# Optimization experiments

Measured on AMD Instinct MI355X. Metric: run time of the kernel, lower is better.

The kernel has to match this reference:

```python
import math
import jax, jax.numpy as jnp
import numpy as np

B, S, H, NH, BS, R = 2, 4096, 1024, 16, 64, 3
HD = H // NH          # 64 head dim
L = S // BS           # 64 blocks
PEN = -10000.0


def _make_rand_attn():
    # data-independent random block plan (like HF bigbird, seeded numpy),
    # per head, per middle query block: R random key blocks excluding
    # global blocks (0, L-1) and the sliding window (i-1, i, i+1)
    rng = np.random.RandomState(42)
    ra = np.zeros((NH, L - 2, R), dtype=np.int64)
    for h in range(NH):
        for i in range(1, L - 1):
            choices = np.array([j for j in range(L) if j not in (0, i - 1, i, i + 1, L - 1)])
            ra[h, i - 1] = rng.choice(choices, R, replace=False)
    return ra


def setup_inputs():
    key = jax.random.key(0)
    ks = jax.random.split(key, 8)
    sc = 1.0 / math.sqrt(H)
    return {
        "Q": jax.random.normal(ks[0], (B, S, H), jnp.float32),
        "K": jax.random.normal(ks[1], (B, S, H), jnp.float32),
        "V": jax.random.normal(ks[2], (B, S, H), jnp.float32),
        "mask": jnp.ones((B, S), jnp.float32),
        "Wq": jax.random.normal(ks[3], (H, H), jnp.float32) * sc,
        "bq": jnp.zeros((H,), jnp.float32),
        "Wk": jax.random.normal(ks[4], (H, H), jnp.float32) * sc,
        "bk": jnp.zeros((H,), jnp.float32),
        "Wv": jax.random.normal(ks[5], (H, H), jnp.float32) * sc,
        "bv": jnp.zeros((H,), jnp.float32),
        "rand_attn": jnp.asarray(_make_rand_attn()),
    }


def _forward(Q, K, V, mask, Wq, bq, Wk, bk, Wv, bv, rand_attn):
    rsd = 1.0 / math.sqrt(HD)
    sm = lambda x: jax.nn.softmax(x, axis=-1)

    def proj(x, W, b):  # torch Linear: x @ W^T + b, then split heads
        return (x @ W.T + b).reshape(B, S, NH, HD).transpose(0, 2, 1, 3)

    q = proj(Q, Wq, bq)  # [B,NH,S,HD]
    k = proj(K, Wk, bk)
    v = proj(V, Wv, bv)
    qb = q.reshape(B, NH, L, BS, HD)
    kb = k.reshape(B, NH, L, BS, HD)
    vb = v.reshape(B, NH, L, BS, HD)

    # ---- masks (derived from padding mask, as in HF create_masks_...) ----
    blocked = mask.reshape(B, L, BS)
    from_mask = mask[:, None, :, None]   # [B,1,S,1]
    to_mask = mask[:, None, None, :]     # [B,1,1,S]
    exp_to = jnp.concatenate([blocked[:, 1:-3], blocked[:, 2:-2], blocked[:, 3:-1]], axis=2)  # [B,L-4,3BS]
    band_mask = jnp.einsum('blq,blk->blqk', blocked[:, 2:-2], exp_to)[:, None]  # [B,1,L-4,BS,3BS]

    ra = jnp.broadcast_to(rand_attn[None], (B, NH, L - 2, R))
    bidx = jnp.arange(B)[:, None, None, None]
    hidx = jnp.arange(NH)[None, :, None, None]
    gk = kb[bidx, hidx, ra].reshape(B, NH, L - 2, R * BS, HD)  # gathered random key blocks
    gv = vb[bidx, hidx, ra].reshape(B, NH, L - 2, R * BS, HD)
    rm = blocked[bidx, ra].reshape(B, NH, L - 2, R * BS)
    rand_mask = jnp.einsum('blq,bhlk->bhlqk', blocked[:, 1:-1], rm)  # [B,NH,L-2,BS,R*BS]

    # ---- first block: dense attention over all keys ----
    p1 = jnp.einsum('bhqd,bhkd->bhqk', qb[:, :, 0], k) * rsd + (1.0 - to_mask) * PEN
    ctx_first = jnp.einsum('bhqk,bhkd->bhqd', sm(p1), v)

    # ---- second block: global(0) + window(1,2) + last + random ----
    k2 = jnp.concatenate([kb[:, :, 0], kb[:, :, 1], kb[:, :, 2], kb[:, :, -1], gk[:, :, 0]], axis=2)
    v2 = jnp.concatenate([vb[:, :, 0], vb[:, :, 1], vb[:, :, 2], vb[:, :, -1], gv[:, :, 0]], axis=2)
    p2 = jnp.einsum('bhqd,bhkd->bhqk', qb[:, :, 1], k2) * rsd
    seq_pad2 = jnp.concatenate([to_mask[..., :3 * BS], to_mask[..., -BS:],
                                jnp.ones((B, 1, 1, R * BS), mask.dtype)], axis=3)
    rand_pad2 = jnp.concatenate([jnp.ones((B, NH, BS, 4 * BS), mask.dtype), rand_mask[:, :, 0]], axis=3)
    p2 = p2 + (1.0 - jnp.minimum(seq_pad2, rand_pad2)) * PEN
    ctx_second = jnp.einsum('bhqk,bhkd->bhqd', sm(p2), v2)

    # ---- middle blocks: band (3 sliding) + random + 2 global ----
    exp_k = jnp.concatenate([kb[:, :, 1:-3], kb[:, :, 2:-2], kb[:, :, 3:-1]], axis=3)  # [B,NH,L-4,3BS,HD]
    exp_v = jnp.concatenate([vb[:, :, 1:-3], vb[:, :, 2:-2], vb[:, :, 3:-1]], axis=3)
    mq = qb[:, :, 2:-2]
    inner = jnp.einsum('bhlqd,bhlkd->bhlqk', mq, exp_k) * rsd + (1.0 - band_mask) * PEN
    randp = jnp.einsum('bhlqd,bhlkd->bhlqk', mq, gk[:, :, 1:-1]) * rsd + (1.0 - rand_mask[:, :, 1:-1]) * PEN
    firstp = jnp.einsum('bhlqd,bhkd->bhlqk', mq, kb[:, :, 0]) * rsd + (1.0 - to_mask[:, :, :, None, :BS]) * PEN
    lastp = jnp.einsum('bhlqd,bhkd->bhlqk', mq, kb[:, :, -1]) * rsd + (1.0 - to_mask[:, :, :, None, -BS:]) * PEN
    w = sm(jnp.concatenate([firstp, inner, randp, lastp], axis=-1))  # [B,NH,L-4,BS,(5+R)*BS]
    ctx_mid = jnp.einsum('bhlqk,bhlkd->bhlqd', w[..., BS:4 * BS], exp_v)
    ctx_mid += jnp.einsum('bhlqk,bhlkd->bhlqd', w[..., 4 * BS:(4 + R) * BS], gv[:, :, 1:-1])
    ctx_mid += jnp.einsum('bhlqk,bhkd->bhlqd', w[..., :BS], vb[:, :, 0])
    ctx_mid += jnp.einsum('bhlqk,bhkd->bhlqd', w[..., -BS:], vb[:, :, -1])

    # ---- second-to-last block ----
    k3 = jnp.concatenate([kb[:, :, 0], kb[:, :, -3], kb[:, :, -2], kb[:, :, -1], gk[:, :, -1]], axis=2)
    v3 = jnp.concatenate([vb[:, :, 0], vb[:, :, -3], vb[:, :, -2], vb[:, :, -1], gv[:, :, -1]], axis=2)
    p3 = jnp.einsum('bhqd,bhkd->bhqk', qb[:, :, -2], k3) * rsd
    seq_pad3 = jnp.concatenate([to_mask[..., :BS], to_mask[..., -3 * BS:],
                                jnp.ones((B, 1, 1, R * BS), mask.dtype)], axis=3)
    rand_pad3 = jnp.concatenate([jnp.ones((B, NH, BS, 4 * BS), mask.dtype), rand_mask[:, :, -1]], axis=3)
    p3 = p3 + (1.0 - jnp.minimum(seq_pad3, rand_pad3)) * PEN
    ctx_seclast = jnp.einsum('bhqk,bhkd->bhqd', sm(p3), v3)

    # ---- last block: dense attention over all keys ----
    p4 = jnp.einsum('bhqd,bhkd->bhqk', qb[:, :, -1], k) * rsd + (1.0 - to_mask) * PEN
    ctx_last = jnp.einsum('bhqk,bhkd->bhqd', sm(p4), v)

    ctx = jnp.concatenate([ctx_first[:, :, None], ctx_second[:, :, None], ctx_mid,
                           ctx_seclast[:, :, None], ctx_last[:, :, None]], axis=2)
    ctx = ctx.reshape(B, NH, S, HD) * from_mask
    return ctx.transpose(0, 2, 1, 3).reshape(B, S, NH * HD)


def reference(Q, K, V, mask, Wq, bq, Wk, bk, Wv, bv, rand_attn):
    return _forward(Q, K, V, mask, Wq, bq, Wk, bk, Wv, bv, rand_attn)
```

## Files before the change

kernel.cpp:

```cpp
#include <hip/hip_runtime.h>
#include <hip/hip_bf16.h>
#include <stdint.h>

#define BB 2
#define SS 4096
#define HH 1024
#define NHh 16
#define HD 64
#define LL 64
#define BS 64
#define RR 3
#define PENf (-10000.0f)

typedef unsigned int uint;
typedef __attribute__((ext_vector_type(8))) short bf16x8;
typedef __attribute__((ext_vector_type(4))) float f32x4;

__device__ __forceinline__ ushort f2bf(float f) {
    union { float f; uint u; } v; v.f = f;
    uint u = v.u;
    return (ushort)((u + 0x7fffu + ((u >> 16) & 1u)) >> 16);
}
__device__ __forceinline__ uint pack_bf(float a, float b) {
    return (uint)f2bf(a) | (((uint)f2bf(b)) << 16);
}
__device__ __forceinline__ uint scale_pair(uint w) {
    float lo = __uint_as_float(w << 16) * 0.125f;
    float hi = __uint_as_float(w & 0xffff0000u) * 0.125f;
    return (uint)f2bf(lo) | (((uint)f2bf(hi)) << 16);
}
__device__ __forceinline__ uint4 scale4(uint4 w) {
    uint4 o;
    o.x = scale_pair(w.x); o.y = scale_pair(w.y);
    o.z = scale_pair(w.z); o.w = scale_pair(w.w);
    return o;
}
__device__ __forceinline__ void async16(const ushort* g, ushort* l) {
    __builtin_amdgcn_global_load_lds((const __attribute__((address_space(1))) uint*)g,
                                     (__attribute__((address_space(3))) uint*)l,
                                     16, 0, 0);
}

__global__ __launch_bounds__(256)
void cvt_kernel(const float* __restrict__ Xq, const float* __restrict__ Xk,
                const float* __restrict__ Xv, const float* __restrict__ Wq,
                const float* __restrict__ Wk, const float* __restrict__ Wv,
                ushort* __restrict__ Xbf, ushort* __restrict__ Wbf)
{
    const size_t XTOT = (size_t)3 * BB * SS * HH;
    const uint u = blockIdx.x * 256 + threadIdx.x;
    const size_t e = (size_t)u * 8;
    const float* src; ushort* dst;
    if (e < XTOT) {
        const int zz = (int)(e >> 23);
        src = (zz == 0 ? Xq : zz == 1 ? Xk : Xv) + (e & ((1u << 23) - 1));
        dst = Xbf + e;
    } else {
        const size_t e2 = e - XTOT;
        const int zz = (int)(e2 >> 20);
        src = (zz == 0 ? Wq : zz == 1 ? Wk : Wv) + (e2 & ((1u << 20) - 1));
        dst = Wbf + e2;
    }
    float4 a = ((const float4*)src)[0];
    float4 c = ((const float4*)src)[1];
    uint4 o;
    o.x = pack_bf(a.x, a.y); o.y = pack_bf(a.z, a.w);
    o.z = pack_bf(c.x, c.y); o.w = pack_bf(c.z, c.w);
    *(uint4*)dst = o;
}

__global__ __launch_bounds__(256)
void gemm3_kernel(const ushort* __restrict__ Xbf, const ushort* __restrict__ Wbf,
                  const float* __restrict__ bq, const float* __restrict__ bk,
                  const float* __restrict__ bv,
                  ushort* __restrict__ qb, ushort* __restrict__ kb,
                  ushort* __restrict__ vbT)
{
    __shared__ __align__(16) ushort smem[128 * 136];
    ushort* As = smem;
    ushort* Bs = smem + 8192;

    const int z = blockIdx.z;
    const ushort* A  = Xbf + (size_t)z * ((size_t)BB * SS * HH);
    const ushort* Bt = Wbf + (size_t)z * (HH * HH);
    const float* bias = (z == 0) ? bq : (z == 1) ? bk : bv;

    const int tid = threadIdx.x;
    const int m0 = blockIdx.x * 128;
    const int n0 = blockIdx.y * 128;
    const int wave = tid >> 6;
    const int lane = tid & 63;
    const int l15 = lane & 15;
    const int quad = lane >> 4;
    const int wr = wave >> 1, wc = wave & 1;

    f32x4 acc[4][4];
#pragma unroll
    for (int i = 0; i < 4; ++i)
#pragma unroll
        for (int j = 0; j < 4; ++j) acc[i][j] = (f32x4){0.f, 0.f, 0.f, 0.f};

    const int p8 = (lane & 3) * 8;
    const ushort* Abase = A + (size_t)(m0 + wave * 32 + (lane >> 2)) * HH + p8;
    const ushort* Bbase = Bt + (size_t)(n0 + wave * 32 + (lane >> 2)) * HH + p8;

#define STAGE_G(k0, bp)                                        \
    do {                                                       \
        ushort* A0 = As + (bp) * 4096 + wave * 1024;           \
        ushort* B0 = Bs + (bp) * 4096 + wave * 1024;           \
        async16(Abase + (k0), A0);                             \
        async16(Abase + 16 * HH + (k0), A0 + 512);             \
        async16(Bbase + (k0), B0);                             \
        async16(Bbase + 16 * HH + (k0), B0 + 512);             \
    } while (0)

    STAGE_G(0, 0);
    for (int k0 = 0, bp = 0; k0 < HH; k0 += 32, bp ^= 1) {
        __syncthreads();
        if (k0 + 32 < HH) STAGE_G(k0 + 32, bp ^ 1);
        bf16x8 af[4], bfr[4];
#pragma unroll
        for (int mt = 0; mt < 4; ++mt)
            af[mt] = *(const bf16x8*)(As + bp * 4096 + (wr * 64 + mt * 16 + l15) * 32 + quad * 8);
#pragma unroll
        for (int nt = 0; nt < 4; ++nt)
            bfr[nt] = *(const bf16x8*)(Bs + bp * 4096 + (wc * 64 + nt * 16 + l15) * 32 + quad * 8);
        if (z < 2) {
#pragma unroll
            for (int i = 0; i < 4; ++i)
#pragma unroll
                for (int j = 0; j < 4; ++j)
                    acc[i][j] = __builtin_amdgcn_mfma_f32_16x16x32_bf16(bfr[i], af[j], acc[i][j], 0, 0, 0);
        } else {
#pragma unroll
            for (int i = 0; i < 4; ++i)
#pragma unroll
                for (int j = 0; j < 4; ++j)
                    acc[i][j] = __builtin_amdgcn_mfma_f32_16x16x32_bf16(af[i], bfr[j], acc[i][j], 0, 0, 0);
        }
    }
#undef STAGE_G

    if (z < 2) {
        ushort* outp = (z == 0) ? qb : kb;
#pragma unroll
        for (int wt = 0; wt < 4; ++wt) {
            const int n_base = n0 + wc * 64 + wt * 16 + quad * 4;
            const float4 b4 = *(const float4*)&bias[n_base];
            const int nh = n_base >> 6;
            const int hd = n_base & 63;
#pragma unroll
            for (int xt = 0; xt < 4; ++xt) {
                const int m = m0 + wr * 64 + xt * 16 + l15;
                const int bgl = m >> 12, s = m & 4095;
                uint2 pk;
                pk.x = pack_bf(acc[wt][xt][0] + b4.x, acc[wt][xt][1] + b4.y);
                pk.y = pack_bf(acc[wt][xt][2] + b4.z, acc[wt][xt][3] + b4.w);
                *(uint2*)&outp[((size_t)((bgl << 4) | nh) * SS + s) * HD + hd] = pk;
            }
        }
    } else {
        __syncthreads();
        ushort* stg = smem;
#pragma unroll
        for (int nt = 0; nt < 4; ++nt) {
            const int n_local = wc * 64 + nt * 16 + l15;
            const float bn = bias[n0 + n_local];
#pragma unroll
            for (int mt = 0; mt < 4; ++mt) {
                const int m_base = wr * 64 + mt * 16 + quad * 4;
                uint2 pk;
                pk.x = pack_bf(acc[mt][nt][0] + bn, acc[mt][nt][1] + bn);
                pk.y = pack_bf(acc[mt][nt][2] + bn, acc[mt][nt][3] + bn);
                *(uint2*)(stg + n_local * 136 + m_base) = pk;
            }
        }
        __syncthreads();
        const int n_row = tid >> 1;
        const int half = tid & 1;
        const int n = n0 + n_row;
        const int nh = n >> 6, hd = n & 63;
        const int bgl = m0 >> 12;
        const int sbase = (m0 & 4095) + half * 64;
        const uint4* src = (const uint4*)(stg + n_row * 136 + half * 64);
        uint4* dst = (uint4*)(vbT + ((size_t)((bgl << 4) | nh) * HD + hd) * SS + sbase);
#pragma unroll
        for (int j = 0; j < 8; ++j) dst[j] = src[j];
    }
}

__global__ __launch_bounds__(256)
void proj3_kernel(const float* __restrict__ Xq, const float* __restrict__ Xk,
                  const float* __restrict__ Xv,
                  const float* __restrict__ Wq, const float* __restrict__ Wk,
                  const float* __restrict__ Wv,
                  const float* __restrict__ bq, const float* __restrict__ bk,
                  const float* __restrict__ bv,
                  ushort* __restrict__ qb, ushort* __restrict__ kb,
                  ushort* __restrict__ vbT)
{
    __shared__ __align__(16) ushort smem[128 * 136];
    ushort* As = smem;
    ushort* Bs = smem + 128 * 40;

    const int z = blockIdx.z;
    const float* X    = (z == 0) ? Xq : (z == 1) ? Xk : Xv;
    const float* W    = (z == 0) ? Wq : (z == 1) ? Wk : Wv;
    const float* bias = (z == 0) ? bq : (z == 1) ? bk : bv;

    const int tid = threadIdx.x;
    const int m0 = blockIdx.x * 128;
    const int n0 = blockIdx.y * 128;
    const int wave = tid >> 6;
    const int lane = tid & 63;
    const int l15 = lane & 15;
    const int quad = lane >> 4;
    const int wr = wave >> 1, wc = wave & 1;

    f32x4 acc[4][4];
#pragma unroll
    for (int mt = 0; mt < 4; ++mt)
#pragma unroll
        for (int nt = 0; nt < 4; ++nt) acc[mt][nt] = (f32x4){0.f, 0.f, 0.f, 0.f};

    const int srow = tid >> 1;
    const int shalf = tid & 1;
    const float* xp = X + (size_t)(m0 + srow) * HH + shalf * 16;
    const float* wp = W + (size_t)(n0 + srow) * HH + shalf * 16;
    ushort* asw = As + srow * 40 + shalf * 16;
    ushort* bsw = Bs + srow * 40 + shalf * 16;

    for (int k0 = 0; k0 < HH; k0 += 32) {
        float4 a0 = *(const float4*)(xp + k0);
        float4 a1 = *(const float4*)(xp + k0 + 4);
        float4 a2 = *(const float4*)(xp + k0 + 8);
        float4 a3 = *(const float4*)(xp + k0 + 12);
        float4 b0 = *(const float4*)(wp + k0);
        float4 b1 = *(const float4*)(wp + k0 + 4);
        float4 b2 = *(const float4*)(wp + k0 + 8);
        float4 b3 = *(const float4*)(wp + k0 + 12);
        __syncthreads();
        uint4 pa, pb;
        pa.x = pack_bf(a0.x, a0.y); pa.y = pack_bf(a0.z, a0.w);
        pa.z = pack_bf(a1.x, a1.y); pa.w = pack_bf(a1.z, a1.w);
        *(uint4*)asw = pa;
        pa.x = pack_bf(a2.x, a2.y); pa.y = pack_bf(a2.z, a2.w);
        pa.z = pack_bf(a3.x, a3.y); pa.w = pack_bf(a3.z, a3.w);
        *(uint4*)(asw + 8) = pa;
        pb.x = pack_bf(b0.x, b0.y); pb.y = pack_bf(b0.z, b0.w);
        pb.z = pack_bf(b1.x, b1.y); pb.w = pack_bf(b1.z, b1.w);
        *(uint4*)bsw = pb;
        pb.x = pack_bf(b2.x, b2.y); pb.y = pack_bf(b2.z, b2.w);
        pb.z = pack_bf(b3.x, b3.y); pb.w = pack_bf(b3.z, b3.w);
        *(uint4*)(bsw + 8) = pb;
        __syncthreads();

        bf16x8 af[4], bfr[4];
#pragma unroll
        for (int mt = 0; mt < 4; ++mt)
            af[mt] = *(const bf16x8*)(As + (wr * 64 + mt * 16 + l15) * 40 + quad * 8);
#pragma unroll
        for (int nt = 0; nt < 4; ++nt)
            bfr[nt] = *(const bf16x8*)(Bs + (wc * 64 + nt * 16 + l15) * 40 + quad * 8);
#pragma unroll
        for (int mt = 0; mt < 4; ++mt)
#pragma unroll
            for (int nt = 0; nt < 4; ++nt)
                acc[mt][nt] = __builtin_amdgcn_mfma_f32_16x16x32_bf16(af[mt], bfr[nt], acc[mt][nt], 0, 0, 0);
    }

    if (z < 2) {
        ushort* outp = (z == 0) ? qb : kb;
#pragma unroll
        for (int nt = 0; nt < 4; ++nt) {
            const int n = n0 + wc * 64 + nt * 16 + l15;
            const float bn = bias[n];
            const int nh = n >> 6, hd = n & 63;
#pragma unroll
            for (int mt = 0; mt < 4; ++mt) {
#pragma unroll
                for (int rr = 0; rr < 4; ++rr) {
                    const int m = m0 + wr * 64 + mt * 16 + quad * 4 + rr;
                    const int bgl = m >> 12, s = m & 4095;
                    outp[((size_t)((bgl << 4) | nh) * SS + s) * HD + hd] = f2bf(acc[mt][nt][rr] + bn);
                }
            }
        }
    } else {
        __syncthreads();
        ushort* stg = smem;
#pragma unroll
        for (int nt = 0; nt < 4; ++nt) {
            const int n_local = wc * 64 + nt * 16 + l15;
            const float bn = bias[n0 + n_local];
#pragma unroll
            for (int mt = 0; mt < 4; ++mt) {
                const int m_base = wr * 64 + mt * 16 + quad * 4;
                uint2 pk;
                pk.x = pack_bf(acc[mt][nt][0] + bn, acc[mt][nt][1] + bn);
                pk.y = pack_bf(acc[mt][nt][2] + bn, acc[mt][nt][3] + bn);
                *(uint2*)(stg + n_local * 136 + m_base) = pk;
            }
        }
        __syncthreads();
        const int n_row = tid >> 1;
        const int half = tid & 1;
        const int n = n0 + n_row;
        const int nh = n >> 6, hd = n & 63;
        const int bgl = m0 >> 12;
        const int sbase = (m0 & 4095) + half * 64;
        const uint4* src = (const uint4*)(stg + n_row * 136 + half * 64);
        uint4* dst = (uint4*)(vbT + ((size_t)((bgl << 4) | nh) * HD + hd) * SS + sbase);
#pragma unroll
        for (int j = 0; j < 8; ++j) dst[j] = src[j];
    }
}

__global__ __launch_bounds__(256)
void attn_kernel(const ushort* __restrict__ qg, const ushort* __restrict__ kg,
                 const ushort* __restrict__ vTg,
                 const float* __restrict__ mask, const int* __restrict__ rand_attn,
                 float* __restrict__ out, float* __restrict__ partO,
                 float* __restrict__ partML)
{
    __shared__ __align__(16) ushort qs_ps[64][72];
    __shared__ __align__(16) ushort ks2[2][2][64][32];
    __shared__ __align__(16) ushort vs2[2][2][64][32];
    __shared__ __align__(16) float qm_s[64];
    __shared__ __align__(16) float km_s[2][64];

    const int tid = threadIdx.x;
    const int wid = blockIdx.x;
    const int bh = wid / 78;
    const int r = wid - bh * 78;
    const int b = bh >> 4, h = bh & 15;

    int i, nkb;
    int kbl[8], pfl[8];
    bool dense;
    int part = 0, which = 0;
    if (r < 62) {
        dense = false;
        i = r + 1;
        const int* ra = rand_attn + ((size_t)h * (LL - 2) + (i - 1)) * RR;
        if (i == 1) {
            kbl[0] = 0; kbl[1] = 1; kbl[2] = 2; kbl[3] = LL - 1;
            kbl[4] = ra[0]; kbl[5] = ra[1]; kbl[6] = ra[2]; kbl[7] = 0;
            pfl[0] = pfl[1] = pfl[2] = pfl[3] = 0;
            pfl[4] = pfl[5] = pfl[6] = 1; pfl[7] = 0;
            nkb = 7;
        } else if (i == LL - 2) {
            kbl[0] = 0; kbl[1] = LL - 3; kbl[2] = LL - 2; kbl[3] = LL - 1;
            kbl[4] = ra[0]; kbl[5] = ra[1]; kbl[6] = ra[2]; kbl[7] = 0;
            pfl[0] = pfl[1] = pfl[2] = pfl[3] = 0;
            pfl[4] = pfl[5] = pfl[6] = 1; pfl[7] = 0;
            nkb = 7;
        } else {
            kbl[0] = 0;      pfl[0] = 0;
            kbl[1] = i - 1;  pfl[1] = 1;
            kbl[2] = i;      pfl[2] = 1;
            kbl[3] = i + 1;  pfl[3] = 1;
            kbl[4] = LL - 1; pfl[4] = 0;
            kbl[5] = ra[0]; kbl[6] = ra[1]; kbl[7] = ra[2];
            pfl[5] = pfl[6] = pfl[7] = 1;
            nkb = 8;
        }
    } else {
        dense = true;
        const int r2 = r - 62;
        which = r2 >> 3;
        part = r2 & 7;
        i = which ? (LL - 1) : 0;
        nkb = 8;
#pragma unroll
        for (int j = 0; j < 8; ++j) { kbl[j] = part * 8 + j; pfl[j] = 0; }
    }

    const int lane = tid & 63;
    const int wave = tid >> 6;
    const int l15 = lane & 15;
    const int quad = lane >> 4;
    const int srow = lane >> 2;
    const int p8 = (lane & 3) * 8;
    const ushort* kgb = kg + (size_t)bh * SS * HD;
    const ushort* vgb = vTg + (size_t)bh * HD * SS;

#define STAGE_KV(kb_, bp)                                                        \
    do {                                                                         \
        const size_t krow = (size_t)((kb_) * BS + wave * 16 + srow) * HD;        \
        async16(kgb + krow + p8,      &ks2[bp][0][wave * 16][0]);                \
        async16(kgb + krow + 32 + p8, &ks2[bp][1][wave * 16][0]);                \
        const size_t vrow = (size_t)(wave * 16 + srow) * SS + (kb_) * BS;        \
        async16(vgb + vrow + p8,      &vs2[bp][0][wave * 16][0]);                \
        async16(vgb + vrow + 32 + p8, &vs2[bp][1][wave * 16][0]);                \
    } while (0)

    {
        const int row = tid >> 2;
        const int c0 = (tid & 3) * 16;
        const ushort* src = qg + ((size_t)bh * SS + i * BS + row) * HD + c0;
        uint4 w0 = *(const uint4*)src;
        uint4 w1 = *(const uint4*)(src + 8);
        *(uint4*)&qs_ps[row][c0] = scale4(w0);
        *(uint4*)&qs_ps[row][c0 + 8] = scale4(w1);
        if (tid < 64) qm_s[tid] = mask[(size_t)b * SS + i * BS + tid];
    }
    STAGE_KV(kbl[0], 0);
    if (tid < 64) km_s[0][tid] = mask[(size_t)b * SS + kbl[0] * BS + tid];
    __syncthreads();

    bf16x8 aq[2];
    aq[0] = *(const bf16x8*)&qs_ps[wave * 16 + l15][quad * 8];
    aq[1] = *(const bf16x8*)&qs_ps[wave * 16 + l15][32 + quad * 8];
    const float qm = qm_s[wave * 16 + l15];

    float mrow = -1e30f, lrow = 0.0f;
    f32x4 accO[4];
#pragma unroll
    for (int dt = 0; dt < 4; ++dt) accO[dt] = (f32x4){0.f, 0.f, 0.f, 0.f};

    for (int it = 0; it < nkb; ++it) {
        const int cur = it & 1;
        if (it + 1 < nkb) {
            STAGE_KV(kbl[it + 1], cur ^ 1);
            if (tid < 64) km_s[cur ^ 1][tid] = mask[(size_t)b * SS + kbl[it + 1] * BS + tid];
        }
        const int pf = pfl[it];

        f32x4 sc[4];
#pragma unroll
        for (int nt = 0; nt < 4; ++nt) sc[nt] = (f32x4){0.f, 0.f, 0.f, 0.f};
#pragma unroll
        for (int c = 0; c < 2; ++c) {
#pragma unroll
            for (int nt = 0; nt < 4; ++nt) {
                bf16x8 af = *(const bf16x8*)&ks2[cur][c][nt * 16 + l15][quad * 8];
                sc[nt] = __builtin_amdgcn_mfma_f32_16x16x32_bf16(af, aq[c], sc[nt], 0, 0, 0);
            }
        }

        float p[4][4];
        float bm = -1e30f;
#pragma unroll
        for (int nt = 0; nt < 4; ++nt) {
            const float4 km4 = *(const float4*)&km_s[cur][nt * 16 + quad * 4];
            const float kmv[4] = {km4.x, km4.y, km4.z, km4.w};
#pragma unroll
            for (int rr = 0; rr < 4; ++rr) {
                const float pm = pf ? (qm * kmv[rr]) : kmv[rr];
                const float sv = sc[nt][rr] + (1.0f - pm) * PENf;
                p[nt][rr] = sv;
                bm = fmaxf(bm, sv);
            }
        }
        bm = fmaxf(bm, __shfl_xor(bm, 16));
        bm = fmaxf(bm, __shfl_xor(bm, 32));
        const float mn = fmaxf(mrow, bm);
        const float alpha = __expf(mrow - mn);
        mrow = mn;
        float ls = 0.0f;
#pragma unroll
        for (int nt = 0; nt < 4; ++nt)
#pragma unroll
            for (int rr = 0; rr < 4; ++rr) {
                p[nt][rr] = __expf(p[nt][rr] - mn);
                ls += p[nt][rr];
            }
        ls += __shfl_xor(ls, 16);
        ls += __shfl_xor(ls, 32);
        lrow = lrow * alpha + ls;

#pragma unroll
        for (int nt = 0; nt < 4; ++nt) {
            uint2 pk;
            pk.x = pack_bf(p[nt][0], p[nt][1]);
            pk.y = pack_bf(p[nt][2], p[nt][3]);
            *(uint2*)&qs_ps[wave * 16 + l15][nt * 16 + quad * 4] = pk;
        }
        float a4[4];
#pragma unroll
        for (int rr = 0; rr < 4; ++rr) a4[rr] = __shfl(alpha, quad * 4 + rr, 64);
#pragma unroll
        for (int dt = 0; dt < 4; ++dt) {
#pragma unroll
            for (int rr = 0; rr < 4; ++rr) accO[dt][rr] *= a4[rr];
        }

#pragma unroll
        for (int c = 0; c < 2; ++c) {
            bf16x8 ap = *(const bf16x8*)&qs_ps[wave * 16 + l15][c * 32 + quad * 8];
#pragma unroll
            for (int dt = 0; dt < 4; ++dt) {
                bf16x8 bvf = *(const bf16x8*)&vs2[cur][c][dt * 16 + l15][quad * 8];
                accO[dt] = __builtin_amdgcn_mfma_f32_16x16x32_bf16(ap, bvf, accO[dt], 0, 0, 0);
            }
        }

        if (it + 1 < nkb) __syncthreads();
    }
#undef STAGE_KV

    if (!dense) {
#pragma unroll
        for (int rr = 0; rr < 4; ++rr) {
            const int qloc = quad * 4 + rr;
            const float lq = __shfl(lrow, qloc, 64);
            const float inv = qm_s[wave * 16 + qloc] / lq;
#pragma unroll
            for (int dt = 0; dt < 4; ++dt) {
                const int d = dt * 16 + l15;
                out[((size_t)b * SS + i * BS + wave * 16 + qloc) * HH + h * HD + d] = accO[dt][rr] * inv;
            }
        }
    } else {
        const int slot = (bh * 2 + which) * 8 + part;
        float* po = partO + (size_t)slot * 4096;
#pragma unroll
        for (int rr = 0; rr < 4; ++rr) {
            const int qrow = wave * 16 + quad * 4 + rr;
#pragma unroll
            for (int dt = 0; dt < 4; ++dt) {
                const int d = dt * 16 + l15;
                po[qrow * 64 + d] = accO[dt][rr];
            }
        }
        if (lane < 16) {
            partML[slot * 128 + wave * 16 + lane] = mrow;
            partML[slot * 128 + 64 + wave * 16 + lane] = lrow;
        }
    }
}

__global__ __launch_bounds__(256)
void combine_kernel(const float* __restrict__ partO, const float* __restrict__ partML,
                    const float* __restrict__ mask, float* __restrict__ out)
{
    const int g = blockIdx.x;
    const int bh = g >> 1, which = g & 1;
    const int b = bh >> 4, h = bh & 15;
    const int i = which ? (LL - 1) : 0;
    const int t = threadIdx.x;
    const int row = t >> 2;
    const int d0 = (t & 3) * 16;
    const int base = g * 8;

    float mp[8], lp[8];
    float M = -1e30f;
#pragma unroll
    for (int p = 0; p < 8; ++p) {
        mp[p] = partML[(base + p) * 128 + row];
        lp[p] = partML[(base + p) * 128 + 64 + row];
        M = fmaxf(M, mp[p]);
    }
    float L = 0.0f, w[8];
#pragma unroll
    for (int p = 0; p < 8; ++p) { w[p] = __expf(mp[p] - M); L += lp[p] * w[p]; }

    float4 o[4];
#pragma unroll
    for (int j = 0; j < 4; ++j) o[j] = make_float4(0.f, 0.f, 0.f, 0.f);
#pragma unroll
    for (int p = 0; p < 8; ++p) {
        const float* po = partO + (size_t)(base + p) * 4096 + row * 64 + d0;
#pragma unroll
        for (int j = 0; j < 4; ++j) {
            float4 v = *(const float4*)(po + j * 4);
            o[j].x = fmaf(w[p], v.x, o[j].x);
            o[j].y = fmaf(w[p], v.y, o[j].y);
            o[j].z = fmaf(w[p], v.z, o[j].z);
            o[j].w = fmaf(w[p], v.w, o[j].w);
        }
    }
    const float fm = mask[(size_t)b * SS + i * BS + row];
    const float inv = fm / L;
    float* dst = out + ((size_t)b * SS + i * BS + row) * HH + h * HD + d0;
#pragma unroll
    for (int j = 0; j < 4; ++j) {
        float4 v;
        v.x = o[j].x * inv; v.y = o[j].y * inv;
        v.z = o[j].z * inv; v.w = o[j].w * inv;
        *(float4*)(dst + j * 4) = v;
    }
}

extern "C" void kernel_launch(void* const* d_in, const int* in_sizes, int n_in,
                              void* d_out, int out_size, void* d_ws, size_t ws_size,
                              hipStream_t stream) {
    (void)in_sizes; (void)n_in; (void)out_size;
    const float* Q    = (const float*)d_in[0];
    const float* K    = (const float*)d_in[1];
    const float* V    = (const float*)d_in[2];
    const float* mask = (const float*)d_in[3];
    const float* Wq   = (const float*)d_in[4];
    const float* bq   = (const float*)d_in[5];
    const float* Wk   = (const float*)d_in[6];
    const float* bk   = (const float*)d_in[7];
    const float* Wv   = (const float*)d_in[8];
    const float* bv   = (const float*)d_in[9];
    const int*   ra   = (const int*)d_in[10];
    float* out = (float*)d_out;

    const size_t qkv = (size_t)BB * NHh * SS * HD;
    ushort* qb  = (ushort*)d_ws;
    ushort* kb  = qb + qkv;
    ushort* vbT = kb + qkv;
    float* partO  = (float*)(vbT + qkv);
    float* partML = partO + (size_t)512 * 4096;
    ushort* Xbf = (ushort*)(partML + (size_t)512 * 128);
    ushort* Wbf = Xbf + 3 * qkv;
    const size_t need = (size_t)((char*)(Wbf + (size_t)3 * HH * HH) - (char*)d_ws);

    if (ws_size >= need) {
        cvt_kernel<<<13824, 256, 0, stream>>>(Q, K, V, Wq, Wk, Wv, Xbf, Wbf);
        gemm3_kernel<<<dim3(64, 8, 3), 256, 0, stream>>>(Xbf, Wbf, bq, bk, bv, qb, kb, vbT);
    } else {
        proj3_kernel<<<dim3(64, 8, 3), 256, 0, stream>>>(Q, K, V, Wq, Wk, Wv, bq, bk, bv,
                                                         qb, kb, vbT);
    }
    attn_kernel<<<dim3(BB * NHh * 78), 256, 0, stream>>>(qb, kb, vbT, mask, ra,
                                                         out, partO, partML);
    combine_kernel<<<dim3(BB * NHh * 2), 256, 0, stream>>>(partO, partML, mask, out);
}
```

Measured before the change: 303.5 us.

## Fuse split-K combine into attention via atomic counter; use exp2 and MFMA row-sums

Folds log2(e) into the Q scale and the mask penalty so the softmax can use exp2f, and turns the mask add into a single fma seeded into the MFMA accumulator. Row sums come from an extra MFMA against a ones vector instead of shuffle reductions. The separate combine kernel is removed on the main path: the last partial block of each dense row group, detected with an atomic counter reset in cvt_kernel, does the merge itself. This saves one launch and some VALU work, at the cost of a threadfence, an atomic, and a serialized tail combine inside the attention kernel.

```diff
diff --git a/kernel.cpp b/kernel.cpp
--- a/kernel.cpp
+++ b/kernel.cpp
@@ -11,6 +11,8 @@
 #define BS 64
 #define RR 3
 #define PENf (-10000.0f)
+#define PEN2f (-14426.950408889634f)
+#define QSCALE (0.125f * 1.44269504088896f)
 
 typedef unsigned int uint;
 typedef __attribute__((ext_vector_type(8))) short bf16x8;
@@ -25,8 +27,8 @@
     return (uint)f2bf(a) | (((uint)f2bf(b)) << 16);
 }
 __device__ __forceinline__ uint scale_pair(uint w) {
-    float lo = __uint_as_float(w << 16) * 0.125f;
-    float hi = __uint_as_float(w & 0xffff0000u) * 0.125f;
+    float lo = __uint_as_float(w << 16) * QSCALE;
+    float hi = __uint_as_float(w & 0xffff0000u) * QSCALE;
     return (uint)f2bf(lo) | (((uint)f2bf(hi)) << 16);
 }
 __device__ __forceinline__ uint4 scale4(uint4 w) {
@@ -45,8 +47,10 @@
 void cvt_kernel(const float* __restrict__ Xq, const float* __restrict__ Xk,
                 const float* __restrict__ Xv, const float* __restrict__ Wq,
                 const float* __restrict__ Wk, const float* __restrict__ Wv,
-                ushort* __restrict__ Xbf, ushort* __restrict__ Wbf)
+                ushort* __restrict__ Xbf, ushort* __restrict__ Wbf,
+                int* __restrict__ ctr)
 {
+    if (blockIdx.x == 0 && threadIdx.x < 64) ctr[threadIdx.x] = 0;
     const size_t XTOT = (size_t)3 * BB * SS * HH;
     const uint u = blockIdx.x * 256 + threadIdx.x;
     const size_t e = (size_t)u * 8;
@@ -321,7 +325,7 @@
                  const ushort* __restrict__ vTg,
                  const float* __restrict__ mask, const int* __restrict__ rand_attn,
                  float* __restrict__ out, float* __restrict__ partO,
-                 float* __restrict__ partML)
+                 float* __restrict__ partML, int* __restrict__ ctr, int fused)
 {
     __shared__ __align__(16) ushort qs_ps[64][72];
     __shared__ __align__(16) ushort ks2[2][2][64][32];
@@ -413,9 +417,19 @@
     aq[0] = *(const bf16x8*)&qs_ps[wave * 16 + l15][quad * 8];
     aq[1] = *(const bf16x8*)&qs_ps[wave * 16 + l15][32 + quad * 8];
     const float qm = qm_s[wave * 16 + l15];
-
-    float mrow = -1e30f, lrow = 0.0f;
+    const float a_pf = qm * (-PEN2f);
+    const float a_nf = -PEN2f;
+
+    bf16x8 ones;
+    {
+        const short ob = (l15 == 0) ? (short)0x3F80 : (short)0;
+#pragma unroll
+        for (int j = 0; j < 8; ++j) ones[j] = ob;
+    }
+
+    float mrow = -1e30f;
     f32x4 accO[4];
+    f32x4 accL = (f32x4){0.f, 0.f, 0.f, 0.f};
 #pragma unroll
     for (int dt = 0; dt < 4; ++dt) accO[dt] = (f32x4){0.f, 0.f, 0.f, 0.f};
 
@@ -429,7 +443,7 @@
 
         f32x4 sc[4];
 #pragma unroll
-        for (int nt = 0; nt < 4; ++nt) sc[nt] = (f32x4){0.f, 0.f, 0.f, 0.f};
+        for (int nt = 0; nt < 4; ++nt) sc[nt] = (f32x4){PEN2f, PEN2f, PEN2f, PEN2f};
 #pragma unroll
         for (int c = 0; c < 2; ++c) {
 #pragma unroll
@@ -439,6 +453,7 @@
             }
         }
 
+        const float a = pf ? a_pf : a_nf;
         float p[4][4];
         float bm = -1e30f;
 #pragma unroll
@@ -447,8 +462,7 @@
             const float kmv[4] = {km4.x, km4.y, km4.z, km4.w};
 #pragma unroll
             for (int rr = 0; rr < 4; ++rr) {
-                const float pm = pf ? (qm * kmv[rr]) : kmv[rr];
-                const float sv = sc[nt][rr] + (1.0f - pm) * PENf;
+                const float sv = fmaf(a, kmv[rr], sc[nt][rr]);
                 p[nt][rr] = sv;
                 bm = fmaxf(bm, sv);
             }
@@ -456,19 +470,13 @@
         bm = fmaxf(bm, __shfl_xor(bm, 16));
         bm = fmaxf(bm, __shfl_xor(bm, 32));
         const float mn = fmaxf(mrow, bm);
-        const float alpha = __expf(mrow - mn);
+        const float alpha = exp2f(mrow - mn);
         mrow = mn;
-        float ls = 0.0f;
 #pragma unroll
         for (int nt = 0; nt < 4; ++nt)
 #pragma unroll
-            for (int rr = 0; rr < 4; ++rr) {
-                p[nt][rr] = __expf(p[nt][rr] - mn);
-                ls += p[nt][rr];
-            }
-        ls += __shfl_xor(ls, 16);
-        ls += __shfl_xor(ls, 32);
-        lrow = lrow * alpha + ls;
+            for (int rr = 0; rr < 4; ++rr)
+                p[nt][rr] = exp2f(p[nt][rr] - mn);
 
 #pragma unroll
         for (int nt = 0; nt < 4; ++nt) {
@@ -481,6 +489,8 @@
 #pragma unroll
         for (int rr = 0; rr < 4; ++rr) a4[rr] = __shfl(alpha, quad * 4 + rr, 64);
 #pragma unroll
+        for (int rr = 0; rr < 4; ++rr) accL[rr] *= a4[rr];
+#pragma unroll
         for (int dt = 0; dt < 4; ++dt) {
 #pragma unroll
             for (int rr = 0; rr < 4; ++rr) accO[dt][rr] *= a4[rr];
@@ -489,6 +499,7 @@
 #pragma unroll
         for (int c = 0; c < 2; ++c) {
             bf16x8 ap = *(const bf16x8*)&qs_ps[wave * 16 + l15][c * 32 + quad * 8];
+            accL = __builtin_amdgcn_mfma_f32_16x16x32_bf16(ap, ones, accL, 0, 0, 0);
 #pragma unroll
             for (int dt = 0; dt < 4; ++dt) {
                 bf16x8 bvf = *(const bf16x8*)&vs2[cur][c][dt * 16 + l15][quad * 8];
@@ -504,7 +515,7 @@
 #pragma unroll
         for (int rr = 0; rr < 4; ++rr) {
             const int qloc = quad * 4 + rr;
-            const float lq = __shfl(lrow, qloc, 64);
+            const float lq = __shfl(accL[rr], quad << 4, 64);
             const float inv = qm_s[wave * 16 + qloc] / lq;
 #pragma unroll
             for (int dt = 0; dt < 4; ++dt) {
@@ -513,7 +524,8 @@
             }
         }
     } else {
-        const int slot = (bh * 2 + which) * 8 + part;
+        const int g = bh * 2 + which;
+        const int slot = g * 8 + part;
         float* po = partO + (size_t)slot * 4096;
 #pragma unroll
         for (int rr = 0; rr < 4; ++rr) {
@@ -524,9 +536,61 @@
                 po[qrow * 64 + d] = accO[dt][rr];
             }
         }
-        if (lane < 16) {
+        if (l15 == 0) {
+#pragma unroll
+            for (int rr = 0; rr < 4; ++rr)
+                partML[slot * 128 + 64 + wave * 16 + quad * 4 + rr] = accL[rr];
+        }
+        if (lane < 16)
             partML[slot * 128 + wave * 16 + lane] = mrow;
-            partML[slot * 128 + 64 + wave * 16 + lane] = lrow;
+
+        if (fused) {
+            __threadfence();
+            __shared__ int last;
+            if (tid == 0) last = (atomicAdd(&ctr[g], 1) == 7);
+            __syncthreads();
+            if (last) {
+                __threadfence();
+                const int row = tid >> 2;
+                const int d0 = (tid & 3) * 16;
+                const int base = g * 8;
+                float mp[8], lp[8];
+                float M = -1e30f;
+#pragma unroll
+                for (int p2 = 0; p2 < 8; ++p2) {
+                    mp[p2] = partML[(base + p2) * 128 + row];
+                    lp[p2] = partML[(base + p2) * 128 + 64 + row];
+                    M = fmaxf(M, mp[p2]);
+                }
+                float L = 0.0f, w[8];
+#pragma unroll
+                for (int p2 = 0; p2 < 8; ++p2) { w[p2] = exp2f(mp[p2] - M); L += lp[p2] * w[p2]; }
+                float4 o[4];
+#pragma unroll
+                for (int j = 0; j < 4; ++j) o[j] = make_float4(0.f, 0.f, 0.f, 0.f);
+#pragma unroll
+                for (int p2 = 0; p2 < 8; ++p2) {
+                    const float* pp = partO + (size_t)(base + p2) * 4096 + row * 64 + d0;
+#pragma unroll
+                    for (int j = 0; j < 4; ++j) {
+                        float4 v = *(const float4*)(pp + j * 4);
+                        o[j].x = fmaf(w[p2], v.x, o[j].x);
+                        o[j].y = fmaf(w[p2], v.y, o[j].y);
+                        o[j].z = fmaf(w[p2], v.z, o[j].z);
+                        o[j].w = fmaf(w[p2], v.w, o[j].w);
+                    }
+                }
+                const float fm = mask[(size_t)b * SS + i * BS + row];
+                const float inv = fm / L;
+                float* dst = out + ((size_t)b * SS + i * BS + row) * HH + h * HD + d0;
+#pragma unroll
+                for (int j = 0; j < 4; ++j) {
+                    float4 v;
+                    v.x = o[j].x * inv; v.y = o[j].y * inv;
+                    v.z = o[j].z * inv; v.w = o[j].w * inv;
+                    *(float4*)(dst + j * 4) = v;
+                }
+            }
         }
     }
 }
@@ -554,7 +618,7 @@
     }
     float L = 0.0f, w[8];
 #pragma unroll
-    for (int p = 0; p < 8; ++p) { w[p] = __expf(mp[p] - M); L += lp[p] * w[p]; }
+    for (int p = 0; p < 8; ++p) { w[p] = exp2f(mp[p] - M); L += lp[p] * w[p]; }
 
     float4 o[4];
 #pragma unroll
@@ -606,18 +670,21 @@
     ushort* vbT = kb + qkv;
     float* partO  = (float*)(vbT + qkv);
     float* partML = partO + (size_t)512 * 4096;
-    ushort* Xbf = (ushort*)(partML + (size_t)512 * 128);
+    int* ctr = (int*)(partML + (size_t)512 * 128);
+    ushort* Xbf = (ushort*)(ctr + 64);
     ushort* Wbf = Xbf + 3 * qkv;
     const size_t need = (size_t)((char*)(Wbf + (size_t)3 * HH * HH) - (char*)d_ws);
 
     if (ws_size >= need) {
-        cvt_kernel<<<13824, 256, 0, stream>>>(Q, K, V, Wq, Wk, Wv, Xbf, Wbf);
+        cvt_kernel<<<13824, 256, 0, stream>>>(Q, K, V, Wq, Wk, Wv, Xbf, Wbf, ctr);
         gemm3_kernel<<<dim3(64, 8, 3), 256, 0, stream>>>(Xbf, Wbf, bq, bk, bv, qb, kb, vbT);
+        attn_kernel<<<dim3(BB * NHh * 78), 256, 0, stream>>>(qb, kb, vbT, mask, ra,
+                                                             out, partO, partML, ctr, 1);
     } else {
         proj3_kernel<<<dim3(64, 8, 3), 256, 0, stream>>>(Q, K, V, Wq, Wk, Wv, bq, bk, bv,
                                                          qb, kb, vbT);
-    }
-    attn_kernel<<<dim3(BB * NHh * 78), 256, 0, stream>>>(qb, kb, vbT, mask, ra,
-                                                         out, partO, partML);
-    combine_kernel<<<dim3(BB * NHh * 2), 256, 0, stream>>>(partO, partML, mask, out);
-}
+        attn_kernel<<<dim3(BB * NHh * 78), 256, 0, stream>>>(qb, kb, vbT, mask, ra,
+                                                             out, partO, partML, ctr, 0);
+        combine_kernel<<<dim3(BB * NHh * 2), 256, 0, stream>>>(partO, partML, mask, out);
+    }
+}
```

New measurement: 425.6 us. 40.2% more time.
